# Performance work log

Measured on AMD Instinct MI355X. Metric: run time of the kernel, lower is better.

The kernel has to match this reference:

```python
import jax, jax.numpy as jnp
import numpy as np
from jax import lax

B, T_SRC, I, H, L, O = 1024, 1024, 64, 512, 64, 1


def _lstm_cell(x, h, c, W_ih, W_hh, b):
    # PyTorch gate order: i, f, g, o. b = b_ih + b_hh (same math).
    gates = x @ W_ih.T + h @ W_hh.T + b  # (B, 4H)
    i, f, g, o = jnp.split(gates, 4, axis=-1)
    c_new = jax.nn.sigmoid(f) * c + jax.nn.sigmoid(i) * jnp.tanh(g)
    h_new = jax.nn.sigmoid(o) * jnp.tanh(c_new)
    return h_new, c_new


def setup_inputs() -> dict:
    key = jax.random.key(0)
    ks = jax.random.split(key, 16)
    s_e = 1.0 / np.sqrt(H)
    inp = {
        "src": jax.random.normal(ks[0], (B, T_SRC, I), dtype=jnp.float32),
        "eps": jax.random.normal(ks[1], (B, L), dtype=jnp.float32),
        "tgt_len": 1024,
        # encoder LSTM
        "W_ih_e": jax.random.uniform(ks[2], (4 * H, I), jnp.float32, -s_e, s_e),
        "W_hh_e": jax.random.uniform(ks[3], (4 * H, H), jnp.float32, -s_e, s_e),
        "b_e": jax.random.uniform(ks[4], (4 * H,), jnp.float32, -s_e, s_e),
        # fc_mu / fc_logvar
        "W_mu": jax.random.uniform(ks[5], (L, H), jnp.float32, -s_e, s_e),
        "b_mu": jax.random.uniform(ks[6], (L,), jnp.float32, -s_e, s_e),
        "W_lv": jax.random.uniform(ks[7], (L, H), jnp.float32, -s_e, s_e),
        "b_lv": jax.random.uniform(ks[8], (L,), jnp.float32, -s_e, s_e),
        # z -> h0, c0
        "W_zh": jax.random.uniform(ks[9], (H, L), jnp.float32, -s_e, s_e),
        "b_zh": jax.random.uniform(ks[10], (H,), jnp.float32, -s_e, s_e),
        "W_zc": jax.random.uniform(ks[11], (H, L), jnp.float32, -s_e, s_e),
        "b_zc": jax.random.uniform(ks[12], (H,), jnp.float32, -s_e, s_e),
        # decoder LSTM + fc_out
        "W_ih_d": jax.random.uniform(ks[13], (4 * H, O), jnp.float32, -s_e, s_e),
        "W_hh_d": jax.random.uniform(ks[14], (4 * H, H), jnp.float32, -s_e, s_e),
        "b_d": jax.random.uniform(ks[15], (4 * H,), jnp.float32, -s_e, s_e),
        "W_out": jax.random.uniform(jax.random.fold_in(key, 100), (O, H), jnp.float32, -s_e, s_e),
        "b_out": jax.random.uniform(jax.random.fold_in(key, 101), (O,), jnp.float32, -s_e, s_e),
    }
    return inp


def reference(src, eps, W_ih_e, W_hh_e, b_e, W_mu, b_mu, W_lv, b_lv,
              W_zh, b_zh, W_zc, b_zc, W_ih_d, W_hh_d, b_d, W_out, b_out,
              tgt_len):
    batch = src.shape[0]
    hid = W_hh_e.shape[1]

    # ---- Encoder: LSTM over src, take final hidden state ----
    def enc_step(carry, x_t):
        h, c = carry
        h, c = _lstm_cell(x_t, h, c, W_ih_e, W_hh_e, b_e)
        return (h, c), None

    h0 = jnp.zeros((batch, hid), src.dtype)
    (h_n, _), _ = lax.scan(enc_step, (h0, h0), jnp.swapaxes(src, 0, 1))

    mu = h_n @ W_mu.T + b_mu          # (B, L)
    logvar = h_n @ W_lv.T + b_lv      # (B, L)

    # ---- Reparameterize ----
    z = mu + eps * jnp.exp(0.5 * logvar)

    h_d = jnp.tanh(z @ W_zh.T + b_zh)
    c_d = jnp.tanh(z @ W_zc.T + b_zc)
    x0 = jnp.zeros((batch, W_ih_d.shape[1]), src.dtype)  # (B, output_size)

    def dec_step(carry, _):
        h, c, x = carry
        h, c = _lstm_cell(x, h, c, W_ih_d, W_hh_d, b_d)
        out = h @ W_out.T + b_out     # (B, O)
        return (h, c, out), out

    _, outs = lax.scan(dec_step, (h_d, c_d, x0), None, length=tgt_len)
    recon = jnp.swapaxes(outs, 0, 1)  # (B, tgt_len, O)
    return recon, mu, logvar
```

## Files before the change

### kernel.cpp

```cpp
#include <hip/hip_runtime.h>


#define NWG  256
#define NTHR 256

typedef __attribute__((ext_vector_type(8))) short short8;
typedef __attribute__((ext_vector_type(4))) float f32x4;
typedef __attribute__((ext_vector_type(4))) unsigned int u32x4;

constexpr int Bt = 1024, Tt = 1024, In = 64, Hn = 512, Ln = 64;
constexpr int KE = In + Hn;
constexpr int BSE = KE + 8;
constexpr int KD = Hn;
constexpr int BSD = KD + 8;
constexpr int HST = 48;
constexpr int LDS_BYTES = 128 * BSE * 2 + 64 * HST * 2;
constexpr int AP_MI = 16 * Hn;

template<bool B> struct BoolC { static constexpr bool value = B; };

__device__ __forceinline__ float bf2f(unsigned short s){
  unsigned u = ((unsigned)s) << 16; float f; __builtin_memcpy(&f, &u, 4); return f;
}
__device__ __forceinline__ unsigned short f2bf(float f){
  unsigned u; __builtin_memcpy(&u, &f, 4);
  u += 0x7FFFu + ((u >> 16) & 1u);
  return (unsigned short)(u >> 16);
}
__device__ __forceinline__ float sigm(float x){ return 1.0f / (1.0f + __expf(-x)); }
__device__ __forceinline__ float tanh_(float x){ float e = __expf(2.0f * x); return 1.0f - 2.0f / (e + 1.0f); }

template<bool SAME, int OFF>
__device__ __forceinline__ u32x4 ldA(const void* p){
  u32x4 r;
  if constexpr (SAME) asm volatile("global_load_dwordx4 %0, %1, off offset:%c2 sc0" : "=&v"(r) : "v"(p), "i"(OFF));
  else                asm volatile("global_load_dwordx4 %0, %1, off offset:%c2 sc0 sc1" : "=&v"(r) : "v"(p), "i"(OFF));
  return r;
}
template<int OFF>
__device__ __forceinline__ u32x4 ldP(const void* p){
  u32x4 r;
  asm volatile("global_load_dwordx4 %0, %1, off offset:%c2" : "=&v"(r) : "v"(p), "i"(OFF));
  return r;
}
template<bool SAME>
__device__ __forceinline__ float ld32w(const void* p){
  float r;
  if constexpr (SAME) asm volatile("global_load_dword %0, %1, off sc0" : "=&v"(r) : "v"(p));
  else                asm volatile("global_load_dword %0, %1, off sc0 sc1" : "=&v"(r) : "v"(p));
  asm volatile("s_waitcnt vmcnt(0)" : "+v"(r));
  return r;
}
template<bool SAME>
__device__ __forceinline__ void st16x(void* p, unsigned v){
  if constexpr (SAME) asm volatile("global_store_short %0, %1, off sc0" :: "v"(p), "v"(v) : "memory");
  else                asm volatile("global_store_short %0, %1, off sc0 sc1" :: "v"(p), "v"(v) : "memory");
}
template<bool SAME>
__device__ __forceinline__ void st32x(void* p, float v){
  if constexpr (SAME) asm volatile("global_store_dword %0, %1, off sc0" :: "v"(p), "v"(v) : "memory");
  else                asm volatile("global_store_dword %0, %1, off sc0 sc1" :: "v"(p), "v"(v) : "memory");
}
template<bool SAME>
__device__ __forceinline__ void st128x(void* p, u32x4 v){
  if constexpr (SAME) asm volatile("global_store_dwordx4 %0, %1, off sc0" :: "v"(p), "v"(v) : "memory");
  else                asm volatile("global_store_dwordx4 %0, %1, off sc0 sc1" :: "v"(p), "v"(v) : "memory");
}
__device__ __forceinline__ void stP32(void* p, float v){
  asm volatile("global_store_dword %0, %1, off" :: "v"(p), "v"(v) : "memory");
}
template<bool SAME>
__device__ __forceinline__ void atomAddF(float* p, float v){
  if constexpr (SAME) asm volatile("global_atomic_add_f32 %0, %1, off" :: "v"(p), "v"(v) : "memory");
  else                asm volatile("global_atomic_add_f32 %0, %1, off sc1" :: "v"(p), "v"(v) : "memory");
}
__device__ __forceinline__ unsigned ldMall(const unsigned* p){
  unsigned r;
  asm volatile("global_load_dword %0, %1, off sc0 sc1" : "=&v"(r) : "v"(p) : "memory");
  asm volatile("s_waitcnt vmcnt(0)" : "+v"(r) :: "memory");
  return r;
}
__device__ __forceinline__ void stMall(unsigned* p, unsigned v){
  asm volatile("global_store_dword %0, %1, off sc0 sc1" :: "v"(p), "v"(v) : "memory");
}

__device__ __forceinline__ void group_sync(unsigned* cnt, unsigned target){
  asm volatile("s_waitcnt vmcnt(0)" ::: "memory");
  __syncthreads();
  if (threadIdx.x == 0){
    __hip_atomic_fetch_add(cnt, 1u, __ATOMIC_RELAXED, __HIP_MEMORY_SCOPE_AGENT);
    while (__hip_atomic_load(cnt, __ATOMIC_RELAXED, __HIP_MEMORY_SCOPE_AGENT) < target)
      __builtin_amdgcn_s_sleep(1);
  }
  __syncthreads();
}

template<bool SAME, int CB>
__device__ __forceinline__ void loadChunk(const unsigned short* a0, const unsigned short* a1,
                                          u32x4 (&d)[4][2]){
  d[0][0] = ldA<SAME, (CB +  0) * 2>(a0);  d[0][1] = ldA<SAME, (CB +  0) * 2>(a1);
  d[1][0] = ldA<SAME, (CB + 32) * 2>(a0);  d[1][1] = ldA<SAME, (CB + 32) * 2>(a1);
  d[2][0] = ldA<SAME, (CB + 64) * 2>(a0);  d[2][1] = ldA<SAME, (CB + 64) * 2>(a1);
  d[3][0] = ldA<SAME, (CB + 96) * 2>(a0);  d[3][1] = ldA<SAME, (CB + 96) * 2>(a1);
}

#define TIEC(C) "+v"(A[C][0][0]), "+v"(A[C][0][1]), "+v"(A[C][1][0]), "+v"(A[C][1][1]), \
                "+v"(A[C][2][0]), "+v"(A[C][2][1]), "+v"(A[C][3][0]), "+v"(A[C][3][1])
#define WAITC(C, N) asm volatile("s_waitcnt vmcnt(" N ")" : TIEC(C))

#define COMPC(C, K0, BS) do{                                                     \
    _Pragma("unroll") for (int ti_ = 0; ti_ < 4; ++ti_){                         \
      short8 a0_ = __builtin_bit_cast(short8, A[C][ti_][0]);                     \
      short8 a1_ = __builtin_bit_cast(short8, A[C][ti_][1]);                     \
      _Pragma("unroll") for (int ni_ = 0; ni_ < 4; ++ni_){                       \
        short8 bv_ = *(const short8*)(bbase + ni_ * 16 * (BS) + (K0) + ti_ * 32);\
        acc[0][ni_] = __builtin_amdgcn_mfma_f32_16x16x32_bf16(a0_, bv_, acc[0][ni_], 0, 0, 0); \
        acc[1][ni_] = __builtin_amdgcn_mfma_f32_16x16x32_bf16(a1_, bv_, acc[1][ni_], 0, 0, 0); \
      } } }while(0)

extern "C" __global__ void __launch_bounds__(NTHR, 1)
vae_fused(const float* __restrict__ src, const float* __restrict__ eps,
          const float* __restrict__ Wih_e, const float* __restrict__ Whh_e, const float* __restrict__ b_e,
          const float* __restrict__ Wmu, const float* __restrict__ bmu,
          const float* __restrict__ Wlv, const float* __restrict__ blv,
          const float* __restrict__ Wzh, const float* __restrict__ bzh,
          const float* __restrict__ Wzc, const float* __restrict__ bzc,
          const float* __restrict__ Wih_d, const float* __restrict__ Whh_d, const float* __restrict__ b_d,
          const float* __restrict__ Wout, const float* __restrict__ bout,
          float* __restrict__ out,
          unsigned* cnt_all, unsigned* xcdbuf,
          unsigned short* hbuf0, unsigned short* hbuf1,
          float* zbuf, float* obuf)
{
  const int tid  = threadIdx.x;
  const int wg   = blockIdx.x;
  const int lane = tid & 63;
  const int wave = tid >> 6;
  const int wm   = wave >> 1, wn = wave & 1;
  const int mt   = wg & 15;
  const int nt   = wg >> 4;
  unsigned* cnt  = cnt_all + mt * 32;
  unsigned bars  = 0;

  extern __shared__ short bpanel[];
  unsigned short* hst = (unsigned short*)(bpanel + 128 * BSE);

  const int l15   = lane & 15;
  const int l4    = lane >> 4;
  const int kq    = l4 * 8;
  const int jcol  = nt * 32 + wn * 16 + l15;
  const int arow0 = mt * 64 + wm * 32 + l15;
  const int brow0 = mt * 64 + wm * 32 + l4 * 4;
  const int srow  = wave * 16 + (lane >> 2);
  const int ssub  = lane & 3;

  unsigned xcc;
  asm volatile("s_getreg_b32 %0, hwreg(HW_REG_XCC_ID)" : "=s"(xcc));
  if (tid == 0) stMall(xcdbuf + mt * 16 + nt, xcc + 1u);
  bars += 16; group_sync(cnt, bars);
  unsigned vx = xcc + 1u;
  if (lane < 16) vx = ldMall(xcdbuf + mt * 16 + lane);
  const bool same_xcd = (__ballot(vx == xcc + 1u) == ~0ull);

  auto body = [&](auto SC){
    constexpr bool SAME = decltype(SC)::value;

    {
      const int idx = nt * NTHR + tid;
      const u32x4 z = {0u, 0u, 0u, 0u};
      st128x<SAME>(hbuf0 + (size_t)(mt * 64 + (idx >> 6)) * Hn + (idx & 63) * 8, z);
    }
    for (int idx = tid; idx < 128 * KE; idx += NTHR){
      int q = idx / KE;
      int k = idx - q * KE;
      int gate = (q >> 4) & 3, jl = q & 15, wnn = (q >> 6) & 1;
      int j = nt * 32 + wnn * 16 + jl;
      int r = gate * Hn + j;
      float w = (k < In) ? Wih_e[r * In + k] : Whh_e[(size_t)r * Hn + (k - In)];
      bpanel[q * BSE + k] = (short)f2bf(w);
    }
    float biasr[4], wihr[4];
    #pragma unroll
    for (int ni = 0; ni < 4; ++ni) biasr[ni] = b_e[ni * Hn + jcol];
    bars += 16; group_sync(cnt, bars);

    float c[2][4] = {{0.f,0.f,0.f,0.f},{0.f,0.f,0.f,0.f}};
    const f32x4 fz = {0.f, 0.f, 0.f, 0.f};
    u32x4 A[4][4][2];

    for (int t = 0; t < Tt; ++t){
      const unsigned short* hs = (t & 1) ? hbuf1 : hbuf0;
      unsigned short*       hd = (t & 1) ? hbuf0 : hbuf1;

      const float* sp0 = src + ((size_t)arow0 * Tt + t) * In + kq;
      const float* sp1 = src + ((size_t)(arow0 + 16) * Tt + t) * In + kq;
      u32x4 sv[2][4];
      sv[0][0] = ldP<0>(sp0); sv[0][1] = ldP<16>(sp0); sv[0][2] = ldP<128>(sp0); sv[0][3] = ldP<144>(sp0);
      sv[1][0] = ldP<0>(sp1); sv[1][1] = ldP<16>(sp1); sv[1][2] = ldP<128>(sp1); sv[1][3] = ldP<144>(sp1);

      const unsigned short* ap0 = hs + (size_t)arow0 * Hn + kq;
      const unsigned short* ap1 = ap0 + AP_MI;
      loadChunk<SAME,   0>(ap0, ap1, A[0]);
      loadChunk<SAME, 128>(ap0, ap1, A[1]);
      loadChunk<SAME, 256>(ap0, ap1, A[2]);
      loadChunk<SAME, 384>(ap0, ap1, A[3]);

      asm volatile("s_waitcnt vmcnt(32)"
        : "+v"(sv[0][0]), "+v"(sv[0][1]), "+v"(sv[0][2]), "+v"(sv[0][3]),
          "+v"(sv[1][0]), "+v"(sv[1][1]), "+v"(sv[1][2]), "+v"(sv[1][3]));
      short8 sa[2][2];
      #pragma unroll
      for (int mi = 0; mi < 2; ++mi){
        f32x4 f0 = __builtin_bit_cast(f32x4, sv[mi][0]);
        f32x4 f1 = __builtin_bit_cast(f32x4, sv[mi][1]);
        f32x4 f2 = __builtin_bit_cast(f32x4, sv[mi][2]);
        f32x4 f3 = __builtin_bit_cast(f32x4, sv[mi][3]);
        short8 a0, a1;
        #pragma unroll
        for (int e = 0; e < 4; ++e){
          a0[e] = (short)f2bf(f0[e]); a0[4 + e] = (short)f2bf(f1[e]);
          a1[e] = (short)f2bf(f2[e]); a1[4 + e] = (short)f2bf(f3[e]);
        }
        sa[mi][0] = a0; sa[mi][1] = a1;
      }

      f32x4 acc[2][4];
      #pragma unroll
      for (int mi = 0; mi < 2; ++mi)
        #pragma unroll
        for (int ni = 0; ni < 4; ++ni) acc[mi][ni] = fz;

      const short* bbase = bpanel + (wn * 64 + l15) * BSE + kq;
      #pragma unroll
      for (int kk = 0; kk < 2; ++kk)
        #pragma unroll
        for (int ni = 0; ni < 4; ++ni){
          short8 bv = *(const short8*)(bbase + ni * 16 * BSE + kk * 32);
          acc[0][ni] = __builtin_amdgcn_mfma_f32_16x16x32_bf16(sa[0][kk], bv, acc[0][ni], 0, 0, 0);
          acc[1][ni] = __builtin_amdgcn_mfma_f32_16x16x32_bf16(sa[1][kk], bv, acc[1][ni], 0, 0, 0);
        }

      WAITC(0, "24"); COMPC(0, In +   0, BSE);
      WAITC(1, "16"); COMPC(1, In + 128, BSE);
      WAITC(2,  "8"); COMPC(2, In + 256, BSE);
      WAITC(3,  "0"); COMPC(3, In + 384, BSE);

      #pragma unroll
      for (int mi = 0; mi < 2; ++mi){
        #pragma unroll
        for (int r = 0; r < 4; ++r){
          float gi = acc[mi][0][r] + biasr[0];
          float gf = acc[mi][1][r] + biasr[1];
          float gg = acc[mi][2][r] + biasr[2];
          float go = acc[mi][3][r] + biasr[3];
          float cn = sigm(gf) * c[mi][r] + sigm(gi) * tanh_(gg);
          c[mi][r] = cn;
          float hn = sigm(go) * tanh_(cn);
          hst[(wm * 32 + mi * 16 + l4 * 4 + r) * HST + wn * 16 + l15] = f2bf(hn);
        }
      }
      __syncthreads();
      {
        u32x4 hv = *(const u32x4*)(hst + srow * HST + ssub * 8);
        st128x<SAME>(hd + (size_t)(mt * 64 + srow) * Hn + nt * 32 + ssub * 8, hv);
      }
      bars += 16; group_sync(cnt, bars);
    }

    {
      const int lt = nt * NTHR + tid;
      const int b  = mt * 64 + (lt >> 6);
      const int l  = lt & 63;
      const unsigned short* hp = hbuf0 + (size_t)b * Hn;
      const float* wmrow = Wmu + l * Hn;
      const float* wlrow = Wlv + l * Hn;
      float smu = 0.f, slv = 0.f;
      for (int jj = 0; jj < Hn; jj += 32){
        u32x4 v0 = ldA<SAME,0>(hp + jj),  v1 = ldA<SAME,16>(hp + jj);
        u32x4 v2 = ldA<SAME,32>(hp + jj), v3 = ldA<SAME,48>(hp + jj);
        asm volatile("s_waitcnt vmcnt(0)" : "+v"(v0), "+v"(v1), "+v"(v2), "+v"(v3));
        short8 h0 = __builtin_bit_cast(short8, v0);
        short8 h1 = __builtin_bit_cast(short8, v1);
        short8 h2 = __builtin_bit_cast(short8, v2);
        short8 h3 = __builtin_bit_cast(short8, v3);
        #pragma unroll
        for (int e = 0; e < 8; ++e){
          float f0 = bf2f((unsigned short)h0[e]), f1 = bf2f((unsigned short)h1[e]);
          float f2 = bf2f((unsigned short)h2[e]), f3 = bf2f((unsigned short)h3[e]);
          smu = __builtin_fmaf(f0, wmrow[jj + e], smu);      slv = __builtin_fmaf(f0, wlrow[jj + e], slv);
          smu = __builtin_fmaf(f1, wmrow[jj + 8 + e], smu);  slv = __builtin_fmaf(f1, wlrow[jj + 8 + e], slv);
          smu = __builtin_fmaf(f2, wmrow[jj + 16 + e], smu); slv = __builtin_fmaf(f2, wlrow[jj + 16 + e], slv);
          smu = __builtin_fmaf(f3, wmrow[jj + 24 + e], smu); slv = __builtin_fmaf(f3, wlrow[jj + 24 + e], slv);
        }
      }
      smu += bmu[l]; slv += blv[l];
      out[(size_t)Bt * Tt + (size_t)b * Ln + l] = smu;
      out[(size_t)Bt * Tt + (size_t)Bt * Ln + (size_t)b * Ln + l] = slv;
      st32x<SAME>(zbuf + (size_t)b * Ln + l, smu + eps[(size_t)b * Ln + l] * __expf(0.5f * slv));
    }
    bars += 16; group_sync(cnt, bars);

    for (int idx = tid; idx < 128 * KD; idx += NTHR){
      int q = idx >> 9, k = idx & 511;
      int gate = (q >> 4) & 3, jl = q & 15, wnn = (q >> 6) & 1;
      int j = nt * 32 + wnn * 16 + jl;
      bpanel[q * BSD + k] = (short)f2bf(Whh_d[(size_t)(gate * Hn + j) * Hn + k]);
    }
    #pragma unroll
    for (int ni = 0; ni < 4; ++ni){
      biasr[ni] = b_d[ni * Hn + jcol];
      wihr[ni]  = Wih_d[ni * Hn + jcol];
    }
    const float woutr = Wout[jcol];
    const float bov   = bout[0];
    #pragma unroll
    for (int mi = 0; mi < 2; ++mi){
      #pragma unroll
      for (int r = 0; r < 4; ++r){
        int b = brow0 + mi * 16 + r;
        const float* zp  = zbuf + (size_t)b * Ln;
        const float* whr = Wzh + jcol * Ln;
        const float* wcr = Wzc + jcol * Ln;
        float sh = bzh[jcol], sc = bzc[jcol];
        for (int e0 = 0; e0 < Ln; e0 += 16){
          u32x4 z0 = ldA<SAME,0>(zp + e0),  z1 = ldA<SAME,16>(zp + e0);
          u32x4 z2 = ldA<SAME,32>(zp + e0), z3 = ldA<SAME,48>(zp + e0);
          asm volatile("s_waitcnt vmcnt(0)" : "+v"(z0), "+v"(z1), "+v"(z2), "+v"(z3));
          f32x4 zf0 = __builtin_bit_cast(f32x4, z0);
          f32x4 zf1 = __builtin_bit_cast(f32x4, z1);
          f32x4 zf2 = __builtin_bit_cast(f32x4, z2);
          f32x4 zf3 = __builtin_bit_cast(f32x4, z3);
          #pragma unroll
          for (int e = 0; e < 4; ++e){
            sh = __builtin_fmaf(zf0[e], whr[e0 + e], sh);      sc = __builtin_fmaf(zf0[e], wcr[e0 + e], sc);
            sh = __builtin_fmaf(zf1[e], whr[e0 + 4 + e], sh);  sc = __builtin_fmaf(zf1[e], wcr[e0 + 4 + e], sc);
            sh = __builtin_fmaf(zf2[e], whr[e0 + 8 + e], sh);  sc = __builtin_fmaf(zf2[e], wcr[e0 + 8 + e], sc);
            sh = __builtin_fmaf(zf3[e], whr[e0 + 12 + e], sh); sc = __builtin_fmaf(zf3[e], wcr[e0 + 12 + e], sc);
          }
        }
        c[mi][r] = tanh_(sc);
        st16x<SAME>(hbuf0 + (size_t)b * Hn + jcol, (unsigned)f2bf(tanh_(sh)));
      }
    }
    if (nt == 0 && tid < 3 * 64)
      st32x<SAME>(obuf + (tid >> 6) * Bt + mt * 64 + (tid & 63), bov);
    bars += 16; group_sync(cnt, bars);

    for (int t = 0; t < Tt; ++t){
      const unsigned short* hs = (t & 1) ? hbuf1 : hbuf0;
      unsigned short*       hd = (t & 1) ? hbuf0 : hbuf1;
      float*       oacc  = obuf + (t % 3) * Bt;
      const float* oread = obuf + ((t + 2) % 3) * Bt;
      float*       orst  = obuf + ((t + 1) % 3) * Bt;

      if (nt == 0){
        if (t > 0 && tid < 64){
          float w = ld32w<SAME>(oread + mt * 64 + tid);
          stP32(out + (size_t)(mt * 64 + tid) * Tt + (t - 1), w);
        }
        if (tid < 64) st32x<SAME>(orst + mt * 64 + tid, bov);
      }

      u32x4 xvv[2];
      xvv[0] = ldA<SAME,  0>(oread + brow0);
      xvv[1] = ldA<SAME, 64>(oread + brow0);

      const unsigned short* ap0 = hs + (size_t)arow0 * Hn + kq;
      const unsigned short* ap1 = ap0 + AP_MI;
      loadChunk<SAME,   0>(ap0, ap1, A[0]);
      loadChunk<SAME, 128>(ap0, ap1, A[1]);
      loadChunk<SAME, 256>(ap0, ap1, A[2]);
      loadChunk<SAME, 384>(ap0, ap1, A[3]);

      f32x4 acc[2][4];
      #pragma unroll
      for (int mi = 0; mi < 2; ++mi)
        #pragma unroll
        for (int ni = 0; ni < 4; ++ni) acc[mi][ni] = fz;

      const short* bbase = bpanel + (wn * 64 + l15) * BSD + kq;
      WAITC(0, "24"); COMPC(0,   0, BSD);
      WAITC(1, "16"); COMPC(1, 128, BSD);
      WAITC(2,  "8"); COMPC(2, 256, BSD);
      WAITC(3,  "0"); COMPC(3, 384, BSD);
      asm volatile("s_waitcnt vmcnt(0)" : "+v"(xvv[0]), "+v"(xvv[1]));
      f32x4 xf0 = __builtin_bit_cast(f32x4, xvv[0]);
      f32x4 xf1 = __builtin_bit_cast(f32x4, xvv[1]);

      #pragma unroll
      for (int mi = 0; mi < 2; ++mi){
        #pragma unroll
        for (int r = 0; r < 4; ++r){
          float x = (t == 0) ? 0.f : (mi == 0 ? xf0[r] : xf1[r]);
          float gi = acc[mi][0][r] + biasr[0] + x * wihr[0];
          float gf = acc[mi][1][r] + biasr[1] + x * wihr[1];
          float gg = acc[mi][2][r] + biasr[2] + x * wihr[2];
          float go = acc[mi][3][r] + biasr[3] + x * wihr[3];
          float cn = sigm(gf) * c[mi][r] + sigm(gi) * tanh_(gg);
          c[mi][r] = cn;
          float hn = sigm(go) * tanh_(cn);
          hst[(wm * 32 + mi * 16 + l4 * 4 + r) * HST + wn * 16 + l15] = f2bf(hn);
          float pv = hn * woutr;
          pv += __shfl_xor(pv, 1);
          pv += __shfl_xor(pv, 2);
          pv += __shfl_xor(pv, 4);
          pv += __shfl_xor(pv, 8);
          if (l15 == 0) atomAddF<SAME>(&oacc[brow0 + mi * 16 + r], pv);
        }
      }
      __syncthreads();
      {
        u32x4 hv = *(const u32x4*)(hst + srow * HST + ssub * 8);
        st128x<SAME>(hd + (size_t)(mt * 64 + srow) * Hn + nt * 32 + ssub * 8, hv);
      }
      bars += 16; group_sync(cnt, bars);
    }
    if (nt == 0 && tid < 64){
      float w = ld32w<SAME>(obuf + 0 * Bt + mt * 64 + tid);
      stP32(out + (size_t)(mt * 64 + tid) * Tt + (Tt - 1), w);
    }
  };

  if (same_xcd) body(BoolC<true>{});
  else          body(BoolC<false>{});
}

extern "C" void kernel_launch(void* const* d_in, const int* in_sizes, int n_in,
                              void* d_out, int out_size, void* d_ws, size_t ws_size,
                              hipStream_t stream){
  (void)in_sizes; (void)n_in; (void)out_size; (void)ws_size;
  const float* src   = (const float*)d_in[0];
  const float* eps   = (const float*)d_in[1];
  const float* Wih_e = (const float*)d_in[3];
  const float* Whh_e = (const float*)d_in[4];
  const float* b_e   = (const float*)d_in[5];
  const float* Wmu   = (const float*)d_in[6];
  const float* bmu   = (const float*)d_in[7];
  const float* Wlv   = (const float*)d_in[8];
  const float* blv   = (const float*)d_in[9];
  const float* Wzh   = (const float*)d_in[10];
  const float* bzh   = (const float*)d_in[11];
  const float* Wzc   = (const float*)d_in[12];
  const float* bzc   = (const float*)d_in[13];
  const float* Wih_d = (const float*)d_in[14];
  const float* Whh_d = (const float*)d_in[15];
  const float* b_d   = (const float*)d_in[16];
  const float* Wout  = (const float*)d_in[17];
  const float* bout  = (const float*)d_in[18];

  char* ws = (char*)d_ws;
  unsigned*       cnt   = (unsigned*)ws;
  unsigned*       xcdb  = (unsigned*)(ws + 2048);
  unsigned short* h0    = (unsigned short*)(ws + 4096);
  unsigned short* h1    = (unsigned short*)(ws + 4096 + 1048576);
  float*          zbuf  = (float*)(ws + 4096 + 2 * 1048576);
  float*          obuf  = (float*)(ws + 4096 + 2 * 1048576 + 262144);

  hipFuncSetAttribute((const void*)vae_fused,
                      hipFuncAttributeMaxDynamicSharedMemorySize, LDS_BYTES);
  (void)hipMemsetAsync(ws, 0, 4096, stream);
  hipLaunchKernelGGL(vae_fused, dim3(NWG), dim3(NTHR), LDS_BYTES, stream,
                     src, eps, Wih_e, Whh_e, b_e, Wmu, bmu, Wlv, blv,
                     Wzh, bzh, Wzc, bzc, Wih_d, Whh_d, b_d, Wout, bout,
                     (float*)d_out, cnt, xcdb, h0, h1, zbuf, obuf);
}
```

Baseline: 16.98 ms.

## Split each batch tile into two half-tiles with split release/acquire barriers

Each workgroup's 64-row batch tile is split into two 32-row halves, each handled in its own phase with separate group counters (cntA, cntB). The combined barrier is split into a release and a later acquire. While one half waits for its peers, the other half's recurrent matmul and gate math can run, hiding inter-workgroup sync latency inside the serial LSTM recurrence. In exchange there are twice as many sync points per timestep, each MFMA batch is smaller, and the spin-wait gains a bounded-iteration escape that could silently break correctness if it ever triggers.

```diff
diff --git a/kernel.cpp b/kernel.cpp
--- a/kernel.cpp
+++ b/kernel.cpp
@@ -13,9 +13,8 @@
 constexpr int BSE = KE + 8;
 constexpr int KD = Hn;
 constexpr int BSD = KD + 8;
-constexpr int HST = 48;
-constexpr int LDS_BYTES = 128 * BSE * 2 + 64 * HST * 2;
-constexpr int AP_MI = 16 * Hn;
+constexpr int HSTn = 40;
+constexpr int LDS_BYTES = 128 * BSE * 2 + 32 * HSTn * 2;
 
 template<bool B> struct BoolC { static constexpr bool value = B; };
 
@@ -69,10 +68,8 @@
 __device__ __forceinline__ void stP32(void* p, float v){
   asm volatile("global_store_dword %0, %1, off" :: "v"(p), "v"(v) : "memory");
 }
-template<bool SAME>
 __device__ __forceinline__ void atomAddF(float* p, float v){
-  if constexpr (SAME) asm volatile("global_atomic_add_f32 %0, %1, off" :: "v"(p), "v"(v) : "memory");
-  else                asm volatile("global_atomic_add_f32 %0, %1, off sc1" :: "v"(p), "v"(v) : "memory");
+  asm volatile("global_atomic_add_f32 %0, %1, off" :: "v"(p), "v"(v) : "memory");
 }
 __device__ __forceinline__ unsigned ldMall(const unsigned* p){
   unsigned r;
@@ -84,38 +81,38 @@
   asm volatile("global_store_dword %0, %1, off sc0 sc1" :: "v"(p), "v"(v) : "memory");
 }
 
-__device__ __forceinline__ void group_sync(unsigned* cnt, unsigned target){
+__device__ __forceinline__ void release(unsigned* cnt){
   asm volatile("s_waitcnt vmcnt(0)" ::: "memory");
   __syncthreads();
-  if (threadIdx.x == 0){
+  if (threadIdx.x == 0)
     __hip_atomic_fetch_add(cnt, 1u, __ATOMIC_RELAXED, __HIP_MEMORY_SCOPE_AGENT);
-    while (__hip_atomic_load(cnt, __ATOMIC_RELAXED, __HIP_MEMORY_SCOPE_AGENT) < target)
+}
+__device__ __forceinline__ void acquire(unsigned* cnt, unsigned target){
+  if (threadIdx.x == 0 && target){
+    int g = 0;
+    while (__hip_atomic_load(cnt, __ATOMIC_RELAXED, __HIP_MEMORY_SCOPE_AGENT) < target){
+      if (++g > (1 << 20)) break;
       __builtin_amdgcn_s_sleep(1);
+    }
   }
   __syncthreads();
 }
 
-template<bool SAME, int CB>
-__device__ __forceinline__ void loadChunk(const unsigned short* a0, const unsigned short* a1,
-                                          u32x4 (&d)[4][2]){
-  d[0][0] = ldA<SAME, (CB +  0) * 2>(a0);  d[0][1] = ldA<SAME, (CB +  0) * 2>(a1);
-  d[1][0] = ldA<SAME, (CB + 32) * 2>(a0);  d[1][1] = ldA<SAME, (CB + 32) * 2>(a1);
-  d[2][0] = ldA<SAME, (CB + 64) * 2>(a0);  d[2][1] = ldA<SAME, (CB + 64) * 2>(a1);
-  d[3][0] = ldA<SAME, (CB + 96) * 2>(a0);  d[3][1] = ldA<SAME, (CB + 96) * 2>(a1);
-}
-
-#define TIEC(C) "+v"(A[C][0][0]), "+v"(A[C][0][1]), "+v"(A[C][1][0]), "+v"(A[C][1][1]), \
-                "+v"(A[C][2][0]), "+v"(A[C][2][1]), "+v"(A[C][3][0]), "+v"(A[C][3][1])
-#define WAITC(C, N) asm volatile("s_waitcnt vmcnt(" N ")" : TIEC(C))
-
-#define COMPC(C, K0, BS) do{                                                     \
+#define LOADC1(C, CB) do{                                  \
+    A[C][0] = ldA<SAME, ((CB) +  0) * 2>(ap);              \
+    A[C][1] = ldA<SAME, ((CB) + 32) * 2>(ap);              \
+    A[C][2] = ldA<SAME, ((CB) + 64) * 2>(ap);              \
+    A[C][3] = ldA<SAME, ((CB) + 96) * 2>(ap); }while(0)
+
+#define TIE1(C) "+v"(A[C][0]), "+v"(A[C][1]), "+v"(A[C][2]), "+v"(A[C][3])
+#define WAITC1(C, N) asm volatile("s_waitcnt vmcnt(" N ")" : TIE1(C))
+
+#define COMPC1(C, K0, BS) do{                                                    \
     _Pragma("unroll") for (int ti_ = 0; ti_ < 4; ++ti_){                         \
-      short8 a0_ = __builtin_bit_cast(short8, A[C][ti_][0]);                     \
-      short8 a1_ = __builtin_bit_cast(short8, A[C][ti_][1]);                     \
+      short8 a_ = __builtin_bit_cast(short8, A[C][ti_]);                         \
       _Pragma("unroll") for (int ni_ = 0; ni_ < 4; ++ni_){                       \
         short8 bv_ = *(const short8*)(bbase + ni_ * 16 * (BS) + (K0) + ti_ * 32);\
-        acc[0][ni_] = __builtin_amdgcn_mfma_f32_16x16x32_bf16(a0_, bv_, acc[0][ni_], 0, 0, 0); \
-        acc[1][ni_] = __builtin_amdgcn_mfma_f32_16x16x32_bf16(a1_, bv_, acc[1][ni_], 0, 0, 0); \
+        acc[ni_] = __builtin_amdgcn_mfma_f32_16x16x32_bf16(a_, bv_, acc[ni_], 0, 0, 0); \
       } } }while(0)
 
 extern "C" __global__ void __launch_bounds__(NTHR, 1)
@@ -128,7 +125,7 @@
           const float* __restrict__ Wih_d, const float* __restrict__ Whh_d, const float* __restrict__ b_d,
           const float* __restrict__ Wout, const float* __restrict__ bout,
           float* __restrict__ out,
-          unsigned* cnt_all, unsigned* xcdbuf,
+          unsigned* cntF_all, unsigned* cntA_all, unsigned* cntB_all, unsigned* xcdbuf,
           unsigned short* hbuf0, unsigned short* hbuf1,
           float* zbuf, float* obuf)
 {
@@ -139,25 +136,23 @@
   const int wm   = wave >> 1, wn = wave & 1;
   const int mt   = wg & 15;
   const int nt   = wg >> 4;
-  unsigned* cnt  = cnt_all + mt * 32;
-  unsigned bars  = 0;
+  unsigned* cntF = cntF_all + mt * 16;
+  unsigned* cntA = cntA_all + mt * 16;
+  unsigned* cntB = cntB_all + mt * 16;
+  unsigned barsF = 0;
 
   extern __shared__ short bpanel[];
   unsigned short* hst = (unsigned short*)(bpanel + 128 * BSE);
 
-  const int l15   = lane & 15;
-  const int l4    = lane >> 4;
-  const int kq    = l4 * 8;
-  const int jcol  = nt * 32 + wn * 16 + l15;
-  const int arow0 = mt * 64 + wm * 32 + l15;
-  const int brow0 = mt * 64 + wm * 32 + l4 * 4;
-  const int srow  = wave * 16 + (lane >> 2);
-  const int ssub  = lane & 3;
+  const int l15 = lane & 15;
+  const int l4  = lane >> 4;
+  const int kq  = l4 * 8;
+  const int jcol = nt * 32 + wn * 16 + l15;
 
   unsigned xcc;
   asm volatile("s_getreg_b32 %0, hwreg(HW_REG_XCC_ID)" : "=s"(xcc));
   if (tid == 0) stMall(xcdbuf + mt * 16 + nt, xcc + 1u);
-  bars += 16; group_sync(cnt, bars);
+  release(cntF); barsF += 16; acquire(cntF, barsF);
   unsigned vx = xcc + 1u;
   if (lane < 16) vx = ldMall(xcdbuf + mt * 16 + lane);
   const bool same_xcd = (__ballot(vx == xcc + 1u) == ~0ull);
@@ -182,90 +177,77 @@
     float biasr[4], wihr[4];
     #pragma unroll
     for (int ni = 0; ni < 4; ++ni) biasr[ni] = b_e[ni * Hn + jcol];
-    bars += 16; group_sync(cnt, bars);
-
-    float c[2][4] = {{0.f,0.f,0.f,0.f},{0.f,0.f,0.f,0.f}};
+    release(cntF); barsF += 16; acquire(cntF, barsF);
+
+    float cA[4] = {0.f,0.f,0.f,0.f}, cB[4] = {0.f,0.f,0.f,0.f};
     const f32x4 fz = {0.f, 0.f, 0.f, 0.f};
-    u32x4 A[4][4][2];
-
-    for (int t = 0; t < Tt; ++t){
+    unsigned needA = 0, needB = 0;
+
+    auto enc_phase = [&](int X, int t, unsigned* cntX, unsigned need, float (&cX)[4]){
+      const int arow = mt * 64 + X * 32 + wm * 16 + l15;
       const unsigned short* hs = (t & 1) ? hbuf1 : hbuf0;
       unsigned short*       hd = (t & 1) ? hbuf0 : hbuf1;
 
-      const float* sp0 = src + ((size_t)arow0 * Tt + t) * In + kq;
-      const float* sp1 = src + ((size_t)(arow0 + 16) * Tt + t) * In + kq;
-      u32x4 sv[2][4];
-      sv[0][0] = ldP<0>(sp0); sv[0][1] = ldP<16>(sp0); sv[0][2] = ldP<128>(sp0); sv[0][3] = ldP<144>(sp0);
-      sv[1][0] = ldP<0>(sp1); sv[1][1] = ldP<16>(sp1); sv[1][2] = ldP<128>(sp1); sv[1][3] = ldP<144>(sp1);
-
-      const unsigned short* ap0 = hs + (size_t)arow0 * Hn + kq;
-      const unsigned short* ap1 = ap0 + AP_MI;
-      loadChunk<SAME,   0>(ap0, ap1, A[0]);
-      loadChunk<SAME, 128>(ap0, ap1, A[1]);
-      loadChunk<SAME, 256>(ap0, ap1, A[2]);
-      loadChunk<SAME, 384>(ap0, ap1, A[3]);
-
-      asm volatile("s_waitcnt vmcnt(32)"
-        : "+v"(sv[0][0]), "+v"(sv[0][1]), "+v"(sv[0][2]), "+v"(sv[0][3]),
-          "+v"(sv[1][0]), "+v"(sv[1][1]), "+v"(sv[1][2]), "+v"(sv[1][3]));
-      short8 sa[2][2];
+      const float* sp = src + ((size_t)arow * Tt + t) * In + kq;
+      u32x4 sv0 = ldP<0>(sp), sv1 = ldP<16>(sp), sv2 = ldP<128>(sp), sv3 = ldP<144>(sp);
+
+      acquire(cntX, need);
+
+      const unsigned short* ap = hs + (size_t)arow * Hn + kq;
+      u32x4 A[4][4];
+      LOADC1(0,   0); LOADC1(1, 128); LOADC1(2, 256); LOADC1(3, 384);
+
+      asm volatile("s_waitcnt vmcnt(16)" : "+v"(sv0), "+v"(sv1), "+v"(sv2), "+v"(sv3));
+      f32x4 f0 = __builtin_bit_cast(f32x4, sv0);
+      f32x4 f1 = __builtin_bit_cast(f32x4, sv1);
+      f32x4 f2 = __builtin_bit_cast(f32x4, sv2);
+      f32x4 f3 = __builtin_bit_cast(f32x4, sv3);
+      short8 sa0, sa1;
       #pragma unroll
-      for (int mi = 0; mi < 2; ++mi){
-        f32x4 f0 = __builtin_bit_cast(f32x4, sv[mi][0]);
-        f32x4 f1 = __builtin_bit_cast(f32x4, sv[mi][1]);
-        f32x4 f2 = __builtin_bit_cast(f32x4, sv[mi][2]);
-        f32x4 f3 = __builtin_bit_cast(f32x4, sv[mi][3]);
-        short8 a0, a1;
-        #pragma unroll
-        for (int e = 0; e < 4; ++e){
-          a0[e] = (short)f2bf(f0[e]); a0[4 + e] = (short)f2bf(f1[e]);
-          a1[e] = (short)f2bf(f2[e]); a1[4 + e] = (short)f2bf(f3[e]);
-        }
-        sa[mi][0] = a0; sa[mi][1] = a1;
-      }
-
-      f32x4 acc[2][4];
-      #pragma unroll
-      for (int mi = 0; mi < 2; ++mi)
-        #pragma unroll
-        for (int ni = 0; ni < 4; ++ni) acc[mi][ni] = fz;
-
+      for (int e = 0; e < 4; ++e){
+        sa0[e] = (short)f2bf(f0[e]); sa0[4 + e] = (short)f2bf(f1[e]);
+        sa1[e] = (short)f2bf(f2[e]); sa1[4 + e] = (short)f2bf(f3[e]);
+      }
+
+      f32x4 acc[4] = {fz, fz, fz, fz};
       const short* bbase = bpanel + (wn * 64 + l15) * BSE + kq;
       #pragma unroll
-      for (int kk = 0; kk < 2; ++kk)
-        #pragma unroll
-        for (int ni = 0; ni < 4; ++ni){
-          short8 bv = *(const short8*)(bbase + ni * 16 * BSE + kk * 32);
-          acc[0][ni] = __builtin_amdgcn_mfma_f32_16x16x32_bf16(sa[0][kk], bv, acc[0][ni], 0, 0, 0);
-          acc[1][ni] = __builtin_amdgcn_mfma_f32_16x16x32_bf16(sa[1][kk], bv, acc[1][ni], 0, 0, 0);
-        }
-
-      WAITC(0, "24"); COMPC(0, In +   0, BSE);
-      WAITC(1, "16"); COMPC(1, In + 128, BSE);
-      WAITC(2,  "8"); COMPC(2, In + 256, BSE);
-      WAITC(3,  "0"); COMPC(3, In + 384, BSE);
+      for (int ni = 0; ni < 4; ++ni){
+        short8 bv0 = *(const short8*)(bbase + ni * 16 * BSE + 0);
+        short8 bv1 = *(const short8*)(bbase + ni * 16 * BSE + 32);
+        acc[ni] = __builtin_amdgcn_mfma_f32_16x16x32_bf16(sa0, bv0, acc[ni], 0, 0, 0);
+        acc[ni] = __builtin_amdgcn_mfma_f32_16x16x32_bf16(sa1, bv1, acc[ni], 0, 0, 0);
+      }
+
+      WAITC1(0, "12"); COMPC1(0, In +   0, BSE);
+      WAITC1(1,  "8"); COMPC1(1, In + 128, BSE);
+      WAITC1(2,  "4"); COMPC1(2, In + 256, BSE);
+      WAITC1(3,  "0"); COMPC1(3, In + 384, BSE);
 
       #pragma unroll
-      for (int mi = 0; mi < 2; ++mi){
-        #pragma unroll
-        for (int r = 0; r < 4; ++r){
-          float gi = acc[mi][0][r] + biasr[0];
-          float gf = acc[mi][1][r] + biasr[1];
-          float gg = acc[mi][2][r] + biasr[2];
-          float go = acc[mi][3][r] + biasr[3];
-          float cn = sigm(gf) * c[mi][r] + sigm(gi) * tanh_(gg);
-          c[mi][r] = cn;
-          float hn = sigm(go) * tanh_(cn);
-          hst[(wm * 32 + mi * 16 + l4 * 4 + r) * HST + wn * 16 + l15] = f2bf(hn);
-        }
+      for (int r = 0; r < 4; ++r){
+        float gi = acc[0][r] + biasr[0];
+        float gf = acc[1][r] + biasr[1];
+        float gg = acc[2][r] + biasr[2];
+        float go = acc[3][r] + biasr[3];
+        float cn = sigm(gf) * cX[r] + sigm(gi) * tanh_(gg);
+        cX[r] = cn;
+        float hn = sigm(go) * tanh_(cn);
+        hst[(wm * 16 + l4 * 4 + r) * HSTn + wn * 16 + l15] = f2bf(hn);
       }
       __syncthreads();
-      {
-        u32x4 hv = *(const u32x4*)(hst + srow * HST + ssub * 8);
-        st128x<SAME>(hd + (size_t)(mt * 64 + srow) * Hn + nt * 32 + ssub * 8, hv);
-      }
-      bars += 16; group_sync(cnt, bars);
-    }
+      if (tid < 128){
+        u32x4 hv = *(const u32x4*)(hst + (tid >> 2) * HSTn + (tid & 3) * 8);
+        st128x<SAME>(hd + (size_t)(mt * 64 + X * 32 + (tid >> 2)) * Hn + nt * 32 + (tid & 3) * 8, hv);
+      }
+      release(cntX);
+    };
+
+    for (int t = 0; t < Tt; ++t){
+      enc_phase(0, t, cntA, needA, cA); needA += 16;
+      enc_phase(1, t, cntB, needB, cB); needB += 16;
+    }
+    release(cntF); barsF += 16; acquire(cntF, barsF);
 
     {
       const int lt = nt * NTHR + tid;
@@ -285,12 +267,12 @@
         short8 h3 = __builtin_bit_cast(short8, v3);
         #pragma unroll
         for (int e = 0; e < 8; ++e){
-          float f0 = bf2f((unsigned short)h0[e]), f1 = bf2f((unsigned short)h1[e]);
-          float f2 = bf2f((unsigned short)h2[e]), f3 = bf2f((unsigned short)h3[e]);
-          smu = __builtin_fmaf(f0, wmrow[jj + e], smu);      slv = __builtin_fmaf(f0, wlrow[jj + e], slv);
-          smu = __builtin_fmaf(f1, wmrow[jj + 8 + e], smu);  slv = __builtin_fmaf(f1, wlrow[jj + 8 + e], slv);
-          smu = __builtin_fmaf(f2, wmrow[jj + 16 + e], smu); slv = __builtin_fmaf(f2, wlrow[jj + 16 + e], slv);
-          smu = __builtin_fmaf(f3, wmrow[jj + 24 + e], smu); slv = __builtin_fmaf(f3, wlrow[jj + 24 + e], slv);
+          float g0 = bf2f((unsigned short)h0[e]), g1 = bf2f((unsigned short)h1[e]);
+          float g2 = bf2f((unsigned short)h2[e]), g3 = bf2f((unsigned short)h3[e]);
+          smu = __builtin_fmaf(g0, wmrow[jj + e], smu);      slv = __builtin_fmaf(g0, wlrow[jj + e], slv);
+          smu = __builtin_fmaf(g1, wmrow[jj + 8 + e], smu);  slv = __builtin_fmaf(g1, wlrow[jj + 8 + e], slv);
+          smu = __builtin_fmaf(g2, wmrow[jj + 16 + e], smu); slv = __builtin_fmaf(g2, wlrow[jj + 16 + e], slv);
+          smu = __builtin_fmaf(g3, wmrow[jj + 24 + e], smu); slv = __builtin_fmaf(g3, wlrow[jj + 24 + e], slv);
         }
       }
       smu += bmu[l]; slv += blv[l];
@@ -298,7 +280,7 @@
       out[(size_t)Bt * Tt + (size_t)Bt * Ln + (size_t)b * Ln + l] = slv;
       st32x<SAME>(zbuf + (size_t)b * Ln + l, smu + eps[(size_t)b * Ln + l] * __expf(0.5f * slv));
     }
-    bars += 16; group_sync(cnt, bars);
+    release(cntF); barsF += 16; acquire(cntF, barsF);
 
     for (int idx = tid; idx < 128 * KD; idx += NTHR){
       int q = idx >> 9, k = idx & 511;
@@ -313,11 +295,11 @@
     }
     const float woutr = Wout[jcol];
     const float bov   = bout[0];
-    #pragma unroll
-    for (int mi = 0; mi < 2; ++mi){
+
+    auto dec_init = [&](int X, float (&cX)[4]){
       #pragma unroll
       for (int r = 0; r < 4; ++r){
-        int b = brow0 + mi * 16 + r;
+        int b = mt * 64 + X * 32 + wm * 16 + l4 * 4 + r;
         const float* zp  = zbuf + (size_t)b * Ln;
         const float* whr = Wzh + jcol * Ln;
         const float* wcr = Wzc + jcol * Ln;
@@ -338,83 +320,82 @@
             sh = __builtin_fmaf(zf3[e], whr[e0 + 12 + e], sh); sc = __builtin_fmaf(zf3[e], wcr[e0 + 12 + e], sc);
           }
         }
-        c[mi][r] = tanh_(sc);
+        cX[r] = tanh_(sc);
         st16x<SAME>(hbuf0 + (size_t)b * Hn + jcol, (unsigned)f2bf(tanh_(sh)));
       }
-    }
+    };
+    dec_init(0, cA);
+    dec_init(1, cB);
     if (nt == 0 && tid < 3 * 64)
       st32x<SAME>(obuf + (tid >> 6) * Bt + mt * 64 + (tid & 63), bov);
-    bars += 16; group_sync(cnt, bars);
-
-    for (int t = 0; t < Tt; ++t){
+    release(cntF); barsF += 16; acquire(cntF, barsF);
+
+    auto dec_phase = [&](int X, int t, unsigned* cntX, unsigned need, float (&cX)[4]){
+      const int arow = mt * 64 + X * 32 + wm * 16 + l15;
+      const int brow = mt * 64 + X * 32 + wm * 16 + l4 * 4;
+      const int rX0  = mt * 64 + X * 32;
       const unsigned short* hs = (t & 1) ? hbuf1 : hbuf0;
       unsigned short*       hd = (t & 1) ? hbuf0 : hbuf1;
       float*       oacc  = obuf + (t % 3) * Bt;
       const float* oread = obuf + ((t + 2) % 3) * Bt;
       float*       orst  = obuf + ((t + 1) % 3) * Bt;
 
+      acquire(cntX, need);
+
       if (nt == 0){
-        if (t > 0 && tid < 64){
-          float w = ld32w<SAME>(oread + mt * 64 + tid);
-          stP32(out + (size_t)(mt * 64 + tid) * Tt + (t - 1), w);
+        if (t > 0 && tid < 32){
+          float w = ld32w<SAME>(oread + rX0 + tid);
+          stP32(out + (size_t)(rX0 + tid) * Tt + (t - 1), w);
         }
-        if (tid < 64) st32x<SAME>(orst + mt * 64 + tid, bov);
-      }
-
-      u32x4 xvv[2];
-      xvv[0] = ldA<SAME,  0>(oread + brow0);
-      xvv[1] = ldA<SAME, 64>(oread + brow0);
-
-      const unsigned short* ap0 = hs + (size_t)arow0 * Hn + kq;
-      const unsigned short* ap1 = ap0 + AP_MI;
-      loadChunk<SAME,   0>(ap0, ap1, A[0]);
-      loadChunk<SAME, 128>(ap0, ap1, A[1]);
-      loadChunk<SAME, 256>(ap0, ap1, A[2]);
-      loadChunk<SAME, 384>(ap0, ap1, A[3]);
-
-      f32x4 acc[2][4];
+        if (tid < 32) st32x<SAME>(orst + rX0 + tid, bov);
+      }
+
+      u32x4 xvv = ldA<SAME, 0>(oread + brow);
+      const unsigned short* ap = hs + (size_t)arow * Hn + kq;
+      u32x4 A[4][4];
+      LOADC1(0,   0); LOADC1(1, 128); LOADC1(2, 256); LOADC1(3, 384);
+
+      f32x4 acc[4] = {fz, fz, fz, fz};
+      const short* bbase = bpanel + (wn * 64 + l15) * BSD + kq;
+      WAITC1(0, "12"); COMPC1(0,   0, BSD);
+      WAITC1(1,  "8"); COMPC1(1, 128, BSD);
+      WAITC1(2,  "4"); COMPC1(2, 256, BSD);
+      WAITC1(3,  "0"); COMPC1(3, 384, BSD);
+      asm volatile("s_waitcnt vmcnt(0)" : "+v"(xvv));
+      f32x4 xf = __builtin_bit_cast(f32x4, xvv);
+
       #pragma unroll
-      for (int mi = 0; mi < 2; ++mi)
-        #pragma unroll
-        for (int ni = 0; ni < 4; ++ni) acc[mi][ni] = fz;
-
-      const short* bbase = bpanel + (wn * 64 + l15) * BSD + kq;
-      WAITC(0, "24"); COMPC(0,   0, BSD);
-      WAITC(1, "16"); COMPC(1, 128, BSD);
-      WAITC(2,  "8"); COMPC(2, 256, BSD);
-      WAITC(3,  "0"); COMPC(3, 384, BSD);
-      asm volatile("s_waitcnt vmcnt(0)" : "+v"(xvv[0]), "+v"(xvv[1]));
-      f32x4 xf0 = __builtin_bit_cast(f32x4, xvv[0]);
-      f32x4 xf1 = __builtin_bit_cast(f32x4, xvv[1]);
-
-      #pragma unroll
-      for (int mi = 0; mi < 2; ++mi){
-        #pragma unroll
-        for (int r = 0; r < 4; ++r){
-          float x = (t == 0) ? 0.f : (mi == 0 ? xf0[r] : xf1[r]);
-          float gi = acc[mi][0][r] + biasr[0] + x * wihr[0];
-          float gf = acc[mi][1][r] + biasr[1] + x * wihr[1];
-          float gg = acc[mi][2][r] + biasr[2] + x * wihr[2];
-          float go = acc[mi][3][r] + biasr[3] + x * wihr[3];
-          float cn = sigm(gf) * c[mi][r] + sigm(gi) * tanh_(gg);
-          c[mi][r] = cn;
-          float hn = sigm(go) * tanh_(cn);
-          hst[(wm * 32 + mi * 16 + l4 * 4 + r) * HST + wn * 16 + l15] = f2bf(hn);
-          float pv = hn * woutr;
-          pv += __shfl_xor(pv, 1);
-          pv += __shfl_xor(pv, 2);
-          pv += __shfl_xor(pv, 4);
-          pv += __shfl_xor(pv, 8);
-          if (l15 == 0) atomAddF<SAME>(&oacc[brow0 + mi * 16 + r], pv);
-        }
+      for (int r = 0; r < 4; ++r){
+        float x = (t == 0) ? 0.f : xf[r];
+        float gi = acc[0][r] + biasr[0] + x * wihr[0];
+        float gf = acc[1][r] + biasr[1] + x * wihr[1];
+        float gg = acc[2][r] + biasr[2] + x * wihr[2];
+        float go = acc[3][r] + biasr[3] + x * wihr[3];
+        float cn = sigm(gf) * cX[r] + sigm(gi) * tanh_(gg);
+        cX[r] = cn;
+        float hn = sigm(go) * tanh_(cn);
+        hst[(wm * 16 + l4 * 4 + r) * HSTn + wn * 16 + l15] = f2bf(hn);
+        float pv = hn * woutr;
+        pv += __shfl_xor(pv, 1);
+        pv += __shfl_xor(pv, 2);
+        pv += __shfl_xor(pv, 4);
+        pv += __shfl_xor(pv, 8);
+        if (l15 == 0) atomAddF(&oacc[brow + r], pv);
       }
       __syncthreads();
-      {
-        u32x4 hv = *(const u32x4*)(hst + srow * HST + ssub * 8);
-        st128x<SAME>(hd + (size_t)(mt * 64 + srow) * Hn + nt * 32 + ssub * 8, hv);
-      }
-      bars += 16; group_sync(cnt, bars);
-    }
+      if (tid < 128){
+        u32x4 hv = *(const u32x4*)(hst + (tid >> 2) * HSTn + (tid & 3) * 8);
+        st128x<SAME>(hd + (size_t)(mt * 64 + X * 32 + (tid >> 2)) * Hn + nt * 32 + (tid & 3) * 8, hv);
+      }
+      release(cntX);
+    };
+
+    for (int t = 0; t < Tt; ++t){
+      dec_phase(0, t, cntA, needA, cA); needA += 16;
+      dec_phase(1, t, cntB, needB, cB); needB += 16;
+    }
+    release(cntF); barsF += 16; acquire(cntF, barsF);
+
     if (nt == 0 && tid < 64){
       float w = ld32w<SAME>(obuf + 0 * Bt + mt * 64 + tid);
       stP32(out + (size_t)(mt * 64 + tid) * Tt + (Tt - 1), w);
@@ -449,8 +430,10 @@
   const float* bout  = (const float*)d_in[18];
 
   char* ws = (char*)d_ws;
-  unsigned*       cnt   = (unsigned*)ws;
-  unsigned*       xcdb  = (unsigned*)(ws + 2048);
+  unsigned*       cntF  = (unsigned*)ws;
+  unsigned*       cntA  = (unsigned*)(ws + 1024);
+  unsigned*       cntB  = (unsigned*)(ws + 2048);
+  unsigned*       xcdb  = (unsigned*)(ws + 3072);
   unsigned short* h0    = (unsigned short*)(ws + 4096);
   unsigned short* h1    = (unsigned short*)(ws + 4096 + 1048576);
   float*          zbuf  = (float*)(ws + 4096 + 2 * 1048576);
@@ -462,5 +445,5 @@
   hipLaunchKernelGGL(vae_fused, dim3(NWG), dim3(NTHR), LDS_BYTES, stream,
                      src, eps, Wih_e, Whh_e, b_e, Wmu, bmu, Wlv, blv,
                      Wzh, bzh, Wzc, bzc, Wih_d, Whh_d, b_d, Wout, bout,
-                     (float*)d_out, cnt, xcdb, h0, h1, zbuf, obuf);
-}
+                     (float*)d_out, cntF, cntA, cntB, xcdb, h0, h1, zbuf, obuf);
+}
```

Result: slower. 17.93 ms (+5.6%).
